# Kernel optimization log

Hardware: AMD Instinct MI355X
Metric: run time of the kernel (lower is better)

## Reference

```python
import jax, jax.numpy as jnp
import numpy as np

B, S, D_IN = 2, 2048, 1024
DIM, H, G = 64, 16, 4  # head dim, num_heads, kv groups


def setup_inputs() -> dict:
    key = jax.random.key(0)
    ks = jax.random.split(key, 9)
    query = jax.random.normal(ks[0], (B, S, D_IN), dtype=jnp.float32)
    key_t = jax.random.normal(ks[1], (B, S, D_IN), dtype=jnp.float32)
    value = jax.random.normal(ks[2], (B, S, D_IN), dtype=jnp.float32)
    # causal mask; masked_fill where mask == 0
    mask = jnp.tril(jnp.ones((S, S), dtype=jnp.int32))[None]  # [1,S,S]
    sc = 1.0 / np.sqrt(D_IN)
    Wq = jax.random.normal(ks[3], (H, D_IN, DIM), dtype=jnp.float32) * sc
    bq = jnp.zeros((H, DIM), dtype=jnp.float32)
    Wk = jax.random.normal(ks[4], (G, D_IN, DIM), dtype=jnp.float32) * sc
    bk = jnp.zeros((G, DIM), dtype=jnp.float32)
    Wv = jax.random.normal(ks[5], (G, D_IN, DIM), dtype=jnp.float32) * sc
    bv = jnp.zeros((G, DIM), dtype=jnp.float32)
    return {"query": query, "key": key_t, "value": value, "mask": mask,
            "Wq": Wq, "bq": bq, "Wk": Wk, "bk": bk, "Wv": Wv, "bv": bv}


def reference(query, key, value, mask, Wq, bq, Wk, bk, Wv, bv):
    # batched per-head projections (replaces the Python loop over heads)
    Q = jnp.einsum('bsd,hde->bhse', query, Wq) + bq[None, :, None, :]   # [B,H,S,E]
    K = jnp.einsum('bsd,gde->bgse', key, Wk) + bk[None, :, None, :]     # [B,G,S,E]
    V = jnp.einsum('bsd,gde->bgse', value, Wv) + bv[None, :, None, :]   # [B,G,S,E]
    # head i uses KV group i % G (as in the original loop)
    g_idx = jnp.arange(H) % G
    Kh = K[:, g_idx]  # [B,H,S,E]
    Vh = V[:, g_idx]
    attn = jnp.einsum('bhqe,bhke->bhqk', Q, Kh) / np.sqrt(DIM)          # [B,H,S,S]
    attn = jnp.where(mask[:, None] == 0, jnp.float32(-1e9), attn)
    p = jax.nn.softmax(attn, axis=-1)
    z = jnp.einsum('bhqk,bhke->bhqe', p, Vh)                             # [B,H,S,E]
    # concat heads along last dim (same order as torch.cat of z_list)
    return z.transpose(0, 2, 1, 3).reshape(B, S, H * DIM)
```

## Files before the change

kernel.cpp:

```cpp
#include <hip/hip_runtime.h>
#include <hip/hip_bf16.h>
#include <math.h>

#define S_LEN 2048
#define DIN   1024
#define NH    16
#define NG    4

typedef short s16x8 __attribute__((ext_vector_type(8)));
typedef float f32x4 __attribute__((ext_vector_type(4)));

__device__ __forceinline__ unsigned short f2bf(float x) {
  union { float f; unsigned u; } v; v.f = x;
  unsigned r = v.u + 0x7FFFu + ((v.u >> 16) & 1u);
  return (unsigned short)(r >> 16);
}
__device__ __forceinline__ unsigned cvtpk(float a, float b) {
  unsigned r;
  asm("v_cvt_pk_bf16_f32 %0, %1, %2" : "=v"(r) : "v"(a), "v"(b));
  return r;
}


__global__ __launch_bounds__(256) void k_cast(
    const float* __restrict__ q, const float* __restrict__ k,
    const float* __restrict__ v, unsigned short* __restrict__ AF) {
  const float* src = (blockIdx.y == 0) ? q : (blockIdx.y == 1) ? k : v;
  unsigned short* dst = AF + (size_t)blockIdx.y * 4194304;
  int flat = blockIdx.x * 256 + threadIdx.x;
  int b = flat >> 18, s = (flat >> 7) & 2047, d0 = (flat & 127) * 8;
  const float* sp = src + (size_t)(b * 2048 + s) * 1024 + d0;
  float4 x = *(const float4*)sp;
  float4 y = *(const float4*)(sp + 4);
  union { s16x8 v; unsigned u[4]; } r;
  r.u[0] = cvtpk(x.x, x.y); r.u[1] = cvtpk(x.z, x.w);
  r.u[2] = cvtpk(y.x, y.y); r.u[3] = cvtpk(y.z, y.w);
  unsigned short* p = dst + (size_t)((b * 128 + (s >> 4)) * 32 + (d0 >> 5)) * 512
                    + (s & 15) * 8 + ((d0 >> 3) & 3) * 128;
  *(s16x8*)p = r.v;
}

__global__ __launch_bounds__(256) void k_wtrans(
    const float* __restrict__ Wq, const float* __restrict__ Wk,
    const float* __restrict__ Wv, unsigned short* __restrict__ WF) {
  __shared__ __align__(16) unsigned short T[64][72];
  const int u = blockIdx.x >> 4, D0 = (blockIdx.x & 15) * 64;
  const int t = threadIdx.x;
  const float* src = (u < 16) ? (Wq + (size_t)u * 65536)
                   : (u < 20) ? (Wk + (size_t)(u - 16) * 65536)
                              : (Wv + (size_t)(u - 20) * 65536);
  const int e4 = (t & 15) * 4, dl = t >> 4;
  #pragma unroll
  for (int p = 0; p < 4; ++p) {
    const int d = p * 16 + dl;
    float4 v = *(const float4*)(src + (size_t)(D0 + d) * 64 + e4);
    T[e4 + 0][d] = f2bf(v.x); T[e4 + 1][d] = f2bf(v.y);
    T[e4 + 2][d] = f2bf(v.z); T[e4 + 3][d] = f2bf(v.w);
  }
  __syncthreads();
  const int j = t & 7;
  #pragma unroll
  for (int p = 0; p < 2; ++p) {
    const int e = p * 32 + (t >> 3);
    unsigned short* dst = WF + (size_t)u * 65536
        + (size_t)((e >> 4) * 32 + (D0 >> 5) + (j >> 2)) * 512
        + (e & 15) * 8 + (j & 3) * 128;
    *(s16x8*)dst = *(const s16x8*)&T[e][j * 8];
  }
}

__global__ __launch_bounds__(256, 2) void k_project(
    const unsigned short* __restrict__ AF,
    const float* __restrict__ bq, const float* __restrict__ bk,
    const float* __restrict__ bv,
    const unsigned short* __restrict__ WF,
    unsigned short* __restrict__ QF,
    unsigned short* __restrict__ KF,
    unsigned short* __restrict__ VF) {
  const int i = blockIdx.x;
  const int strip = i & 7, rr = i >> 3;
  const int b = rr / 24, u = rr % 24;
  const int tid = threadIdx.x;
  const int w = tid >> 6, lane = tid & 63, lq = lane & 15, gq = lane >> 4;

  const unsigned short* AFp = AF
      + (size_t)((u < 16) ? 0 : (u < 20) ? 1 : 2) * 4194304
      + (size_t)b * 2097152;
  const float* bias = (u < 16) ? bq + u * 64
                    : (u < 20) ? bk + (u - 16) * 64 : bv + (u - 20) * 64;
  const unsigned short* WFp = WF + (size_t)u * 65536;
  const int sb0 = strip * 16 + w * 4;

  f32x4 acc[4][4] = {};
  #pragma unroll 2
  for (int dk = 0; dk < 32; ++dk) {
    s16x8 a[4], bf[4];
    #pragma unroll
    for (int rf = 0; rf < 4; ++rf)
      a[rf] = *(const s16x8*)(AFp + (size_t)((sb0 + rf) * 32 + dk) * 512 + lane * 8);
    #pragma unroll
    for (int n = 0; n < 4; ++n)
      bf[n] = *(const s16x8*)(WFp + (size_t)(n * 32 + dk) * 512 + lane * 8);
    #pragma unroll
    for (int rf = 0; rf < 4; ++rf)
      #pragma unroll
      for (int n = 0; n < 4; ++n)
        acc[rf][n] = __builtin_amdgcn_mfma_f32_16x16x32_bf16(a[rf], bf[n], acc[rf][n], 0, 0, 0);
  }

  float bvv[4];
  #pragma unroll
  for (int n = 0; n < 4; ++n) bvv[n] = bias[n * 16 + lq];

  unsigned short* dst = (u < 16) ? QF + (size_t)(b * 16 + u) * 131072
                      : (u < 20) ? KF + (size_t)(b * 4 + (u - 16)) * 131072
                                 : VF + (size_t)(b * 4 + (u - 20)) * 131072;
  #pragma unroll
  for (int rf = 0; rf < 4; ++rf)
    #pragma unroll
    for (int n = 0; n < 4; ++n)
      #pragma unroll
      for (int r = 0; r < 4; ++r) {
        const int s = strip * 256 + w * 64 + rf * 16 + gq * 4 + r;
        const int d = n * 16 + lq;
        const unsigned short hv = f2bf(acc[rf][n][r] + bvv[n]);
        if (u < 20)
          dst[(size_t)((s >> 4) * 2 + (d >> 5)) * 512
              + (s & 15) * 8 + ((d >> 3) & 3) * 128 + (d & 7)] = hv;
        else
          dst[(size_t)(n * 64 + (s >> 5)) * 512
              + lq * 8 + ((s >> 3) & 3) * 128 + (s & 7)] = hv;
      }
}

__global__ __launch_bounds__(64, 2) void k_attn(
    const unsigned short* __restrict__ QF, const unsigned short* __restrict__ KF,
    const unsigned short* __restrict__ VF, float* __restrict__ out) {
  __shared__ __align__(16) unsigned short P[16][72];
  const int lane = threadIdx.x, lq = lane & 15, gq = lane >> 4;
  const int bidx = blockIdx.x;
  const int lid = (bidx & 7) * 128 + (bidx >> 3);
  const int pr = lid & 63, h = lid >> 6;
  const int b = blockIdx.y, g = h & 3;

  const unsigned short* QFp = QF + (size_t)(b * NH + h) * 131072;
  const unsigned short* KFp = KF + (size_t)(b * NG + g) * 131072;
  const unsigned short* VFp = VF + (size_t)(b * NG + g) * 131072;
  float* outp = out + (size_t)b * S_LEN * 1024 + h * 64;
  const float SC = 0.1803368801111204f;

  auto process = [&](int j) {
    const int ntiles = (j >> 2) + 1;
    const s16x8 qf0 = *(const s16x8*)(QFp + (size_t)(j * 2 + 0) * 512 + lane * 8);
    const s16x8 qf1 = *(const s16x8*)(QFp + (size_t)(j * 2 + 1) * 512 + lane * 8);
    f32x4 z[4] = {};
    float m = -INFINITY, l = 0.f;

    auto loadK = [&](s16x8 (&A)[4], s16x8 (&B)[4], int t) {
      #pragma unroll
      for (int f = 0; f < 4; ++f) {
        const unsigned short* kp = KFp + (size_t)((t * 4 + f) * 2) * 512 + lane * 8;
        A[f] = *(const s16x8*)kp;
        B[f] = *(const s16x8*)(kp + 512);
      }
    };

    auto tile = [&](const s16x8 (&kA)[4], const s16x8 (&kB)[4], int t) {
      const int k0 = t * 64;
      s16x8 vb[4][2];
      #pragma unroll
      for (int n = 0; n < 4; ++n)
        #pragma unroll
        for (int ks = 0; ks < 2; ++ks)
          vb[n][ks] = *(const s16x8*)(VFp + (size_t)(n * 64 + t * 2 + ks) * 512 + lane * 8);
      f32x4 sv[4];
      __builtin_amdgcn_s_setprio(1);
      #pragma unroll
      for (int f = 0; f < 4; ++f) {
        f32x4 s = {};
        s = __builtin_amdgcn_mfma_f32_16x16x32_bf16(kA[f], qf0, s, 0, 0, 0);
        s = __builtin_amdgcn_mfma_f32_16x16x32_bf16(kB[f], qf1, s, 0, 0, 0);
        sv[f] = s;
      }
      __builtin_amdgcn_s_setprio(0);
      #pragma unroll
      for (int f = 0; f < 4; ++f)
        #pragma unroll
        for (int r = 0; r < 4; ++r) sv[f][r] *= SC;
      if (t == ntiles - 1) {
        const int qrow = j * 16 + lq;
        #pragma unroll
        for (int f = 0; f < 4; ++f)
          #pragma unroll
          for (int r = 0; r < 4; ++r)
            if (k0 + f * 16 + gq * 4 + r > qrow) sv[f][r] = -1e30f;
      }
      float mf[4];
      #pragma unroll
      for (int f = 0; f < 4; ++f)
        mf[f] = fmaxf(fmaxf(sv[f][0], sv[f][1]), fmaxf(sv[f][2], sv[f][3]));
      float pm = fmaxf(fmaxf(mf[0], mf[1]), fmaxf(mf[2], mf[3]));
      pm = fmaxf(pm, __shfl_xor(pm, 16));
      pm = fmaxf(pm, __shfl_xor(pm, 32));
      if (__any(pm - m > 8.f)) {
        const float mn = fmaxf(m, pm);
        const float sc = __builtin_amdgcn_exp2f(m - mn);
        m = mn; l *= sc;
        #pragma unroll
        for (int r = 0; r < 4; ++r) {
          float scr = __shfl(sc, gq * 4 + r, 64);
          z[0][r] *= scr; z[1][r] *= scr; z[2][r] *= scr; z[3][r] *= scr;
        }
      }
      float s0 = 0.f, s1 = 0.f;
      #pragma unroll
      for (int f = 0; f < 4; ++f) {
        float p0 = __builtin_amdgcn_exp2f(sv[f][0] - m);
        float p1 = __builtin_amdgcn_exp2f(sv[f][1] - m);
        float p2 = __builtin_amdgcn_exp2f(sv[f][2] - m);
        float p3 = __builtin_amdgcn_exp2f(sv[f][3] - m);
        s0 += p0 + p1; s1 += p2 + p3;
        *(uint2*)&P[lq][f * 16 + gq * 4] = make_uint2(cvtpk(p0, p1), cvtpk(p2, p3));
      }
      float ss = s0 + s1;
      ss += __shfl_xor(ss, 16);
      ss += __shfl_xor(ss, 32);
      l += ss;
      s16x8 pa[2];
      #pragma unroll
      for (int ks = 0; ks < 2; ++ks)
        pa[ks] = *(const s16x8*)&P[lq][ks * 32 + gq * 8];
      __builtin_amdgcn_s_setprio(1);
      #pragma unroll
      for (int n = 0; n < 4; ++n)
        #pragma unroll
        for (int ks = 0; ks < 2; ++ks)
          z[n] = __builtin_amdgcn_mfma_f32_16x16x32_bf16(pa[ks], vb[n][ks], z[n], 0, 0, 0);
      __builtin_amdgcn_s_setprio(0);
    };

    s16x8 cA[4], cB[4], nA[4], nB[4];
    loadK(cA, cB, 0);
    int t = 0;
    while (true) {
      loadK(nA, nB, (t + 1 < ntiles) ? t + 1 : t);
      tile(cA, cB, t);
      if (++t >= ntiles) break;
      loadK(cA, cB, (t + 1 < ntiles) ? t + 1 : t);
      tile(nA, nB, t);
      if (++t >= ntiles) break;
    }

    #pragma unroll
    for (int r = 0; r < 4; ++r) {
      float lr = __shfl(l, gq * 4 + r, 64);
      float inv = __builtin_amdgcn_rcpf(lr);
      float* op = outp + (size_t)(j * 16 + gq * 4 + r) * 1024;
      #pragma unroll
      for (int n = 0; n < 4; ++n) op[n * 16 + lq] = z[n][r] * inv;
    }
  };

  process(pr);
  process(127 - pr);
}

extern "C" void kernel_launch(void* const* d_in, const int* in_sizes, int n_in,
                              void* d_out, int out_size, void* d_ws, size_t ws_size,
                              hipStream_t stream) {
  const float* query = (const float*)d_in[0];
  const float* key   = (const float*)d_in[1];
  const float* value = (const float*)d_in[2];
  const float* Wq = (const float*)d_in[4];
  const float* bq = (const float*)d_in[5];
  const float* Wk = (const float*)d_in[6];
  const float* bk = (const float*)d_in[7];
  const float* Wv = (const float*)d_in[8];
  const float* bv = (const float*)d_in[9];
  float* out = (float*)d_out;

  unsigned short* AF = (unsigned short*)d_ws;
  unsigned short* WF = AF + 12582912;
  unsigned short* QF = WF + 1572864;
  unsigned short* KF = QF + 4194304;
  unsigned short* VF = KF + 1048576;

  hipLaunchKernelGGL(k_cast, dim3(2048, 3), dim3(256), 0, stream,
                     query, key, value, AF);
  hipLaunchKernelGGL(k_wtrans, dim3(384), dim3(256), 0, stream, Wq, Wk, Wv, WF);
  hipLaunchKernelGGL(k_project, dim3(384), dim3(256), 0, stream,
                     AF, bq, bk, bv, WF, QF, KF, VF);
  hipLaunchKernelGGL(k_attn, dim3(1024, 2), dim3(64), 0, stream, QF, KF, VF, out);
}
```

Baseline: 100.8 us.

## Group four heads sharing a KV group per block and fold softmax scale into Q

```diff
diff --git a/kernel.cpp b/kernel.cpp
--- a/kernel.cpp
+++ b/kernel.cpp
@@ -90,6 +90,7 @@
                     : (u < 20) ? bk + (u - 16) * 64 : bv + (u - 20) * 64;
   const unsigned short* WFp = WF + (size_t)u * 65536;
   const int sb0 = strip * 16 + w * 4;
+  const float OSC = (u < 16) ? 0.1803368801111204f : 1.0f;
 
   f32x4 acc[4][4] = {};
   #pragma unroll 2
@@ -123,7 +124,7 @@
       for (int r = 0; r < 4; ++r) {
         const int s = strip * 256 + w * 64 + rf * 16 + gq * 4 + r;
         const int d = n * 16 + lq;
-        const unsigned short hv = f2bf(acc[rf][n][r] + bvv[n]);
+        const unsigned short hv = f2bf((acc[rf][n][r] + bvv[n]) * OSC);
         if (u < 20)
           dst[(size_t)((s >> 4) * 2 + (d >> 5)) * 512
               + (s & 15) * 8 + ((d >> 3) & 3) * 128 + (d & 7)] = hv;
@@ -133,136 +134,129 @@
       }
 }
 
-__global__ __launch_bounds__(64, 2) void k_attn(
+__global__ __launch_bounds__(256) void k_attn(
     const unsigned short* __restrict__ QF, const unsigned short* __restrict__ KF,
     const unsigned short* __restrict__ VF, float* __restrict__ out) {
-  __shared__ __align__(16) unsigned short P[16][72];
-  const int lane = threadIdx.x, lq = lane & 15, gq = lane >> 4;
-  const int bidx = blockIdx.x;
-  const int lid = (bidx & 7) * 128 + (bidx >> 3);
-  const int pr = lid & 63, h = lid >> 6;
-  const int b = blockIdx.y, g = h & 3;
+  __shared__ __align__(16) unsigned short P[4][16][72];
+  const int tid = threadIdx.x;
+  const int w = tid >> 6, lane = tid & 63, lq = lane & 15, gq = lane >> 4;
+  const int x = blockIdx.x;
+  const int xcd = x & 7, li = x >> 3;
+  const int g = xcd & 3;
+  const int j = 127 - (li * 2 + (xcd >> 2));
+  const int h = g + 4 * w;
+  const int b = blockIdx.y;
 
   const unsigned short* QFp = QF + (size_t)(b * NH + h) * 131072;
   const unsigned short* KFp = KF + (size_t)(b * NG + g) * 131072;
   const unsigned short* VFp = VF + (size_t)(b * NG + g) * 131072;
-  float* outp = out + (size_t)b * S_LEN * 1024 + h * 64;
-  const float SC = 0.1803368801111204f;
-
-  auto process = [&](int j) {
-    const int ntiles = (j >> 2) + 1;
-    const s16x8 qf0 = *(const s16x8*)(QFp + (size_t)(j * 2 + 0) * 512 + lane * 8);
-    const s16x8 qf1 = *(const s16x8*)(QFp + (size_t)(j * 2 + 1) * 512 + lane * 8);
-    f32x4 z[4] = {};
-    float m = -INFINITY, l = 0.f;
-
-    auto loadK = [&](s16x8 (&A)[4], s16x8 (&B)[4], int t) {
-      #pragma unroll
-      for (int f = 0; f < 4; ++f) {
-        const unsigned short* kp = KFp + (size_t)((t * 4 + f) * 2) * 512 + lane * 8;
-        A[f] = *(const s16x8*)kp;
-        B[f] = *(const s16x8*)(kp + 512);
-      }
-    };
-
-    auto tile = [&](const s16x8 (&kA)[4], const s16x8 (&kB)[4], int t) {
-      const int k0 = t * 64;
-      s16x8 vb[4][2];
-      #pragma unroll
-      for (int n = 0; n < 4; ++n)
-        #pragma unroll
-        for (int ks = 0; ks < 2; ++ks)
-          vb[n][ks] = *(const s16x8*)(VFp + (size_t)(n * 64 + t * 2 + ks) * 512 + lane * 8);
-      f32x4 sv[4];
-      __builtin_amdgcn_s_setprio(1);
-      #pragma unroll
-      for (int f = 0; f < 4; ++f) {
-        f32x4 s = {};
-        s = __builtin_amdgcn_mfma_f32_16x16x32_bf16(kA[f], qf0, s, 0, 0, 0);
-        s = __builtin_amdgcn_mfma_f32_16x16x32_bf16(kB[f], qf1, s, 0, 0, 0);
-        sv[f] = s;
-      }
-      __builtin_amdgcn_s_setprio(0);
+  const int nt = (j >> 2) + 1;
+
+  const s16x8 qf0 = *(const s16x8*)(QFp + (size_t)(j * 2 + 0) * 512 + lane * 8);
+  const s16x8 qf1 = *(const s16x8*)(QFp + (size_t)(j * 2 + 1) * 512 + lane * 8);
+  f32x4 z[4] = {};
+  float m = -INFINITY, l = 0.f;
+
+  auto loadK = [&](s16x8 (&A)[4], s16x8 (&B)[4], int t) {
+    #pragma unroll
+    for (int f = 0; f < 4; ++f) {
+      const unsigned short* kp = KFp + (size_t)((t * 4 + f) * 2) * 512 + lane * 8;
+      A[f] = *(const s16x8*)kp;
+      B[f] = *(const s16x8*)(kp + 512);
+    }
+  };
+
+  auto tile = [&](const s16x8 (&kA)[4], const s16x8 (&kB)[4], int t) {
+    const int k0 = t * 64;
+    s16x8 vb[4][2];
+    #pragma unroll
+    for (int n = 0; n < 4; ++n)
+      #pragma unroll
+      for (int ks = 0; ks < 2; ++ks)
+        vb[n][ks] = *(const s16x8*)(VFp + (size_t)(n * 64 + t * 2 + ks) * 512 + lane * 8);
+    f32x4 sv[4];
+    __builtin_amdgcn_s_setprio(1);
+    #pragma unroll
+    for (int f = 0; f < 4; ++f) {
+      f32x4 s = {};
+      s = __builtin_amdgcn_mfma_f32_16x16x32_bf16(kA[f], qf0, s, 0, 0, 0);
+      s = __builtin_amdgcn_mfma_f32_16x16x32_bf16(kB[f], qf1, s, 0, 0, 0);
+      sv[f] = s;
+    }
+    __builtin_amdgcn_s_setprio(0);
+    if (t == nt - 1) {
+      const int qrow = j * 16 + lq;
       #pragma unroll
       for (int f = 0; f < 4; ++f)
         #pragma unroll
-        for (int r = 0; r < 4; ++r) sv[f][r] *= SC;
-      if (t == ntiles - 1) {
-        const int qrow = j * 16 + lq;
-        #pragma unroll
-        for (int f = 0; f < 4; ++f)
-          #pragma unroll
-          for (int r = 0; r < 4; ++r)
-            if (k0 + f * 16 + gq * 4 + r > qrow) sv[f][r] = -1e30f;
+        for (int r = 0; r < 4; ++r)
+          if (k0 + f * 16 + gq * 4 + r > qrow) sv[f][r] = -1e30f;
+    }
+    float mf[4];
+    #pragma unroll
+    for (int f = 0; f < 4; ++f)
+      mf[f] = fmaxf(fmaxf(sv[f][0], sv[f][1]), fmaxf(sv[f][2], sv[f][3]));
+    float pm = fmaxf(fmaxf(mf[0], mf[1]), fmaxf(mf[2], mf[3]));
+    pm = fmaxf(pm, __shfl_xor(pm, 16));
+    pm = fmaxf(pm, __shfl_xor(pm, 32));
+    if (__any(pm - m > 8.f)) {
+      const float mn = fmaxf(m, pm);
+      const float sc = __builtin_amdgcn_exp2f(m - mn);
+      m = mn; l *= sc;
+      #pragma unroll
+      for (int r = 0; r < 4; ++r) {
+        float scr = __shfl(sc, gq * 4 + r, 64);
+        z[0][r] *= scr; z[1][r] *= scr; z[2][r] *= scr; z[3][r] *= scr;
       }
-      float mf[4];
-      #pragma unroll
-      for (int f = 0; f < 4; ++f)
-        mf[f] = fmaxf(fmaxf(sv[f][0], sv[f][1]), fmaxf(sv[f][2], sv[f][3]));
-      float pm = fmaxf(fmaxf(mf[0], mf[1]), fmaxf(mf[2], mf[3]));
-      pm = fmaxf(pm, __shfl_xor(pm, 16));
-      pm = fmaxf(pm, __shfl_xor(pm, 32));
-      if (__any(pm - m > 8.f)) {
-        const float mn = fmaxf(m, pm);
-        const float sc = __builtin_amdgcn_exp2f(m - mn);
-        m = mn; l *= sc;
-        #pragma unroll
-        for (int r = 0; r < 4; ++r) {
-          float scr = __shfl(sc, gq * 4 + r, 64);
-          z[0][r] *= scr; z[1][r] *= scr; z[2][r] *= scr; z[3][r] *= scr;
-        }
-      }
-      float s0 = 0.f, s1 = 0.f;
-      #pragma unroll
-      for (int f = 0; f < 4; ++f) {
-        float p0 = __builtin_amdgcn_exp2f(sv[f][0] - m);
-        float p1 = __builtin_amdgcn_exp2f(sv[f][1] - m);
-        float p2 = __builtin_amdgcn_exp2f(sv[f][2] - m);
-        float p3 = __builtin_amdgcn_exp2f(sv[f][3] - m);
-        s0 += p0 + p1; s1 += p2 + p3;
-        *(uint2*)&P[lq][f * 16 + gq * 4] = make_uint2(cvtpk(p0, p1), cvtpk(p2, p3));
-      }
-      float ss = s0 + s1;
-      ss += __shfl_xor(ss, 16);
-      ss += __shfl_xor(ss, 32);
-      l += ss;
-      s16x8 pa[2];
+    }
+    float s0 = 0.f, s1 = 0.f;
+    #pragma unroll
+    for (int f = 0; f < 4; ++f) {
+      float p0 = __builtin_amdgcn_exp2f(sv[f][0] - m);
+      float p1 = __builtin_amdgcn_exp2f(sv[f][1] - m);
+      float p2 = __builtin_amdgcn_exp2f(sv[f][2] - m);
+      float p3 = __builtin_amdgcn_exp2f(sv[f][3] - m);
+      s0 += p0 + p1; s1 += p2 + p3;
+      *(uint2*)&P[w][lq][f * 16 + gq * 4] = make_uint2(cvtpk(p0, p1), cvtpk(p2, p3));
+    }
+    float ss = s0 + s1;
+    ss += __shfl_xor(ss, 16);
+    ss += __shfl_xor(ss, 32);
+    l += ss;
+    s16x8 pa[2];
+    #pragma unroll
+    for (int ks = 0; ks < 2; ++ks)
+      pa[ks] = *(const s16x8*)&P[w][lq][ks * 32 + gq * 8];
+    __builtin_amdgcn_s_setprio(1);
+    #pragma unroll
+    for (int n = 0; n < 4; ++n)
       #pragma unroll
       for (int ks = 0; ks < 2; ++ks)
-        pa[ks] = *(const s16x8*)&P[lq][ks * 32 + gq * 8];
-      __builtin_amdgcn_s_setprio(1);
-      #pragma unroll
-      for (int n = 0; n < 4; ++n)
-        #pragma unroll
-        for (int ks = 0; ks < 2; ++ks)
-          z[n] = __builtin_amdgcn_mfma_f32_16x16x32_bf16(pa[ks], vb[n][ks], z[n], 0, 0, 0);
-      __builtin_amdgcn_s_setprio(0);
-    };
-
-    s16x8 cA[4], cB[4], nA[4], nB[4];
-    loadK(cA, cB, 0);
-    int t = 0;
-    while (true) {
-      loadK(nA, nB, (t + 1 < ntiles) ? t + 1 : t);
-      tile(cA, cB, t);
-      if (++t >= ntiles) break;
-      loadK(cA, cB, (t + 1 < ntiles) ? t + 1 : t);
-      tile(nA, nB, t);
-      if (++t >= ntiles) break;
-    }
-
-    #pragma unroll
-    for (int r = 0; r < 4; ++r) {
-      float lr = __shfl(l, gq * 4 + r, 64);
-      float inv = __builtin_amdgcn_rcpf(lr);
-      float* op = outp + (size_t)(j * 16 + gq * 4 + r) * 1024;
-      #pragma unroll
-      for (int n = 0; n < 4; ++n) op[n * 16 + lq] = z[n][r] * inv;
-    }
+        z[n] = __builtin_amdgcn_mfma_f32_16x16x32_bf16(pa[ks], vb[n][ks], z[n], 0, 0, 0);
+    __builtin_amdgcn_s_setprio(0);
   };
 
-  process(pr);
-  process(127 - pr);
+  s16x8 cA[4], cB[4], nA[4], nB[4];
+  loadK(cA, cB, 0);
+  int t = 0;
+  while (true) {
+    loadK(nA, nB, (t + 1 < nt) ? t + 1 : t);
+    tile(cA, cB, t);
+    if (++t >= nt) break;
+    loadK(cA, cB, (t + 1 < nt) ? t + 1 : t);
+    tile(nA, nB, t);
+    if (++t >= nt) break;
+  }
+
+  float* outp = out + (size_t)b * S_LEN * 1024 + h * 64;
+  #pragma unroll
+  for (int r = 0; r < 4; ++r) {
+    float lr = __shfl(l, gq * 4 + r, 64);
+    float inv = __builtin_amdgcn_rcpf(lr);
+    float* op = outp + (size_t)(j * 16 + gq * 4 + r) * 1024;
+    #pragma unroll
+    for (int n = 0; n < 4; ++n) op[n * 16 + lq] = z[n][r] * inv;
+  }
 }
 
 extern "C" void kernel_launch(void* const* d_in, const int* in_sizes, int n_in,
@@ -290,5 +284,5 @@
   hipLaunchKernelGGL(k_wtrans, dim3(384), dim3(256), 0, stream, Wq, Wk, Wv, WF);
   hipLaunchKernelGGL(k_project, dim3(384), dim3(256), 0, stream,
                      AF, bq, bk, bv, WF, QF, KF, VF);
-  hipLaunchKernelGGL(k_attn, dim3(1024, 2), dim3(64), 0, stream, QF, KF, VF, out);
-}
+  hipLaunchKernelGGL(k_attn, dim3(512, 2), dim3(256), 0, stream, QF, KF, VF, out);
+}
```

Result: faster. 92.53 us (-8.2%).
